# Optimization experiments

Hardware: AMD Instinct MI355X
Metric: run time of the kernel (lower is better)

Reference implementation:

```python
import jax, jax.numpy as jnp
import numpy as np

B, S, D, H = 2, 2048, 1024, 16
DK = D // H  # 64
SQRT_DK = DK ** 0.5
NEG = -1e9


def setup_inputs() -> dict:
    key = jax.random.key(0)
    ks = jax.random.split(key, 7)
    scale = 1.0 / np.sqrt(D)
    return {
        "x": jax.random.normal(ks[0], (B, S, D), jnp.float32),
        "encoder_output": jax.random.normal(ks[1], (B, S, D), jnp.float32),
        "mask": jax.random.randint(ks[2], (B, S), 0, 2, jnp.int32),
        "WQ": jax.random.normal(ks[3], (D, D), jnp.float32) * scale,
        "WK": jax.random.normal(ks[4], (D, D), jnp.float32) * scale,
        "WV": jax.random.normal(ks[5], (D, D), jnp.float32) * scale,
        "WO": jax.random.normal(ks[6], (D, D), jnp.float32) * scale,
    }


def reference(x, encoder_output, mask, WQ, WK, WV, WO):
    b, s, d = x.shape
    # project and split heads: (b, h, s, dk)
    q = (x @ WQ).reshape(b, s, H, DK).transpose(0, 2, 1, 3)
    k = (encoder_output @ WK).reshape(b, s, H, DK).transpose(0, 2, 1, 3)
    v = (encoder_output @ WV).reshape(b, s, H, DK).transpose(0, 2, 1, 3)
    # scores: (b, h, s_q, s_k)
    scores = jnp.einsum('bhqd,bhkd->bhqk', q, k) / SQRT_DK
    # future mask (strict upper triangle) + padding mask broadcast over key dim
    future = jnp.triu(jnp.ones((s, s), jnp.int32), 1)  # (s, s)
    m = mask[:, None, :, None] + future[None, None, :, :]  # (b, 1->h, s_q, s_k)
    scores = jnp.where(m != 0, NEG, scores)
    attn = jax.nn.softmax(scores, axis=-1)
    # context: (b, s, h, dk) -> (b, s, d)
    ctx = jnp.einsum('bhqk,bhkd->bqhd', attn, v).reshape(b, s, d)
    return ctx @ WO
```

## Files before the change

kernel.cpp:

```cpp
#include <hip/hip_runtime.h>
#include <hip/hip_bf16.h>

constexpr int B = 2, S = 2048, D = 1024, H = 16, DK = 64;
constexpr int M = B * S;
constexpr float LOG2E = 1.44269504088896f;
constexpr float NEGBIG = -3.0e38f;
constexpr float QSCALE = 0.125f * LOG2E;

using short8 = __attribute__((ext_vector_type(8))) short;
using short4v = __attribute__((ext_vector_type(4))) short;
using f32x4 = __attribute__((ext_vector_type(4))) float;

#define GLOBAL_AS __attribute__((address_space(1)))
#define LDS_AS __attribute__((address_space(3)))

__device__ __forceinline__ void gll16(const void* g, void* l) {
  __builtin_amdgcn_global_load_lds((const GLOBAL_AS void*)g, (LDS_AS void*)l, 16, 0, 0);
}

__device__ __forceinline__ short f2bf(float f) {
  __hip_bfloat16 h = __float2bfloat16(f);
  short s;
  __builtin_memcpy(&s, &h, 2);
  return s;
}
__device__ __forceinline__ unsigned pack2bf(float a, float b) {
  return (unsigned)(unsigned short)f2bf(a) | ((unsigned)(unsigned short)f2bf(b) << 16);
}

__global__ __launch_bounds__(256) void prep_kernel(const float* __restrict__ x,
                                                   const float* __restrict__ enc,
                                                   const float* __restrict__ W0,
                                                   const float* __restrict__ W1,
                                                   const float* __restrict__ W2,
                                                   const float* __restrict__ W3,
                                                   short* __restrict__ xb,
                                                   short* __restrict__ encb,
                                                   short* __restrict__ Wt) {
  __shared__ float t[64][65];
  const int bx = blockIdx.x;
  if (bx < 8192) {
    const float4* src = (const float4*)((bx & 4096) ? enc : x);
    short4v* dst = (short4v*)((bx & 4096) ? encb : xb);
    const int i = (bx & 4095) * 256 + threadIdx.x;
    const float4 v = src[i];
    short4v o;
    o[0] = f2bf(v.x); o[1] = f2bf(v.y); o[2] = f2bf(v.z); o[3] = f2bf(v.w);
    dst[i] = o;
  } else {
    const int idx = bx - 8192;
    const int z = idx >> 8, rem = idx & 255;
    const float* W = z == 0 ? W0 : z == 1 ? W1 : z == 2 ? W2 : W3;
    short* dstw = Wt + (size_t)z * D * D;
    const int n0 = (rem & 15) * 64, k0 = (rem >> 4) * 64;
    const int lx = threadIdx.x & 63, ly = threadIdx.x >> 6;
    #pragma unroll
    for (int r = 0; r < 64; r += 4)
      t[r + ly][lx] = W[(size_t)(k0 + r + ly) * D + n0 + lx];
    __syncthreads();
    #pragma unroll
    for (int r = 0; r < 64; r += 4)
      dstw[(size_t)(n0 + r + ly) * D + k0 + lx] = f2bf(t[lx][r + ly]);
  }
}

__global__ __launch_bounds__(512, 2) void gemm_qkv_kernel(const short* __restrict__ A0,
                                                          const short* __restrict__ A1,
                                                          const short* __restrict__ Wts,
                                                          short* __restrict__ Cv,
                                                          float* __restrict__ vsum) {
  __shared__ short As[2][4][256][8];
  __shared__ short Bs[2][4][256][8];
  const int z = blockIdx.z;
  const short* __restrict__ A = z ? A1 : A0;
  const short* __restrict__ Bt = Wts + (size_t)z * D * D;
  const float oscale = (z == 0) ? QSCALE : 1.0f;

  const int tid = threadIdx.x;
  const int lane = tid & 63, wid = tid >> 6;
  const int l15 = lane & 15, lg = lane >> 4;
  const int row0 = blockIdx.x * 256, col0 = blockIdx.y * 256;
  const int wm = wid >> 2, wn = wid & 3;
  f32x4 acc[8][4] = {};

  auto stage = [&](int k0, int nb) {
    #pragma unroll
    for (int it = 0; it < 2; ++it) {
      const int c = tid + it * 512;
      const int row = c & 255, kc2 = c >> 8;
      gll16(&A[(size_t)(row0 + row) * D + k0 + kc2 * 8],
            (char*)As + nb * 16384 + kc2 * 4096 + row * 16);
      gll16(&Bt[(size_t)(col0 + row) * D + k0 + kc2 * 8],
            (char*)Bs + nb * 16384 + kc2 * 4096 + row * 16);
    }
  };

  stage(0, 0);
  __syncthreads();
  int cur = 0;
  for (int t = 0; t < D / 32; ++t) {
    if (t < D / 32 - 1) stage((t + 1) * 32, cur ^ 1);
    short8 af[8], bfr[4];
    #pragma unroll
    for (int m = 0; m < 8; ++m) af[m] = *(const short8*)&As[cur][lg][wm * 128 + m * 16 + l15][0];
    #pragma unroll
    for (int n = 0; n < 4; ++n) bfr[n] = *(const short8*)&Bs[cur][lg][wn * 64 + n * 16 + l15][0];
    #pragma unroll
    for (int m = 0; m < 8; ++m)
      #pragma unroll
      for (int n = 0; n < 4; ++n)
        acc[m][n] = __builtin_amdgcn_mfma_f32_16x16x32_bf16(af[m], bfr[n], acc[m][n], 0, 0, 0);
    __syncthreads();
    cur ^= 1;
  }
  #pragma unroll
  for (int m = 0; m < 8; ++m) {
    #pragma unroll
    for (int r = 0; r < 4; ++r) {
      const int row = row0 + wm * 128 + m * 16 + 4 * lg + r;
      #pragma unroll
      for (int n = 0; n < 4; ++n) {
        const int col = col0 + wn * 64 + n * 16 + l15;
        Cv[(size_t)z * M * D + (size_t)row * D + col] = f2bf(acc[m][n][r] * oscale);
      }
    }
  }
  if (z == 2) {
    const int bidx = row0 >> 11;
    #pragma unroll
    for (int n = 0; n < 4; ++n) {
      float s = 0.f;
      #pragma unroll
      for (int m = 0; m < 8; ++m)
        s += acc[m][n][0] + acc[m][n][1] + acc[m][n][2] + acc[m][n][3];
      s += __shfl_xor(s, 16);
      s += __shfl_xor(s, 32);
      if (lg == 0) atomicAdd(&vsum[(size_t)bidx * D + col0 + wn * 64 + n * 16 + l15], s);
    }
  }
}

__global__ __launch_bounds__(256) void gemmO_kernel(const short* __restrict__ A,
                                                    const short* __restrict__ Bt,
                                                    float* __restrict__ C) {
  __shared__ short As[2][4][128][8];
  __shared__ short Bs[2][4][64][8];
  const int tid = threadIdx.x;
  const int lane = tid & 63, wid = tid >> 6;
  const int l15 = lane & 15, lg = lane >> 4;
  const int row0 = blockIdx.x * 128, col0 = blockIdx.y * 64;
  const int wm = wid >> 1, wn = wid & 1;
  f32x4 acc[4][2] = {};

  auto stage = [&](int k0, int nb) {
    #pragma unroll
    for (int it = 0; it < 2; ++it) {
      const int c = tid + it * 256;
      const int row = c & 127, kc2 = c >> 7;
      gll16(&A[(size_t)(row0 + row) * D + k0 + kc2 * 8],
            (char*)As + nb * 8192 + (wid * 64 + it * 256) * 16);
    }
    gll16(&Bt[(size_t)(col0 + lane) * D + k0 + wid * 8],
          (char*)Bs + nb * 4096 + wid * 1024);
  };

  stage(0, 0);
  __syncthreads();
  int cur = 0;
  for (int t = 0; t < D / 32; ++t) {
    if (t < D / 32 - 1) stage((t + 1) * 32, cur ^ 1);
    short8 af[4], bfr[2];
    #pragma unroll
    for (int m = 0; m < 4; ++m) af[m] = *(const short8*)&As[cur][lg][wm * 64 + m * 16 + l15][0];
    #pragma unroll
    for (int n = 0; n < 2; ++n) bfr[n] = *(const short8*)&Bs[cur][lg][wn * 32 + n * 16 + l15][0];
    #pragma unroll
    for (int m = 0; m < 4; ++m)
      #pragma unroll
      for (int n = 0; n < 2; ++n)
        acc[m][n] = __builtin_amdgcn_mfma_f32_16x16x32_bf16(af[m], bfr[n], acc[m][n], 0, 0, 0);
    __syncthreads();
    cur ^= 1;
  }
  #pragma unroll
  for (int m = 0; m < 4; ++m)
    #pragma unroll
    for (int r = 0; r < 4; ++r) {
      const int row = row0 + wm * 64 + m * 16 + 4 * lg + r;
      #pragma unroll
      for (int n = 0; n < 2; ++n)
        C[(size_t)row * D + col0 + wn * 32 + n * 16 + l15] = acc[m][n][r];
    }
}

__device__ __forceinline__ int keyof(int c, int i) {
  return ((c >> 1) << 5) + ((i >> 2) << 3) + ((c & 1) << 2) + (i & 3);
}
__device__ __forceinline__ int vt_byte(int kc, int d, int ksb) {
  return kc * 1024 + ((d ^ (kc & 7)) << 4) + ksb * 2;
}

__global__ __launch_bounds__(512, 4) void attn_kernel(const short* __restrict__ Qb,
                                                      const short* __restrict__ Kb,
                                                      const short* __restrict__ Vb,
                                                      const int* __restrict__ maskp,
                                                      const float* __restrict__ vsum,
                                                      short* __restrict__ ctxb) {
  __shared__ char KsBuf[2][16384];
  __shared__ char VtBuf[2][16384];
  const int bid = blockIdx.x;
  const int qt = (bid < 256) ? 15 - (bid >> 5) : (bid >> 5) - 8;
  const int bh = bid & 31;
  const int b = bh >> 4, h = bh & 15;
  const int tid = threadIdx.x, lane = tid & 63, wid = tid >> 6;
  const int l15 = lane & 15, lg = lane >> 4;
  const int ql = wid * 16 + l15;

  short8 qf[2];
  {
    const size_t o = (size_t)(b * S + qt * 128 + ql) * D + h * DK;
    qf[0] = *(const short8*)&Qb[o + lg * 8];
    qf[1] = *(const short8*)&Qb[o + 32 + lg * 8];
  }
  float m = NEGBIG, l = 0.f;
  f32x4 cx[4] = {};

  const int kkey = keyof(lg, l15);
  const int vu = tid & 63, dv = tid >> 6;
  const int vh = vu >> 5, vl = vu & 31;
  const int vkc = vl >> 2, vksb = (vl & 3) * 2;

  auto stageK = [&](int jc, int nb) {
    const size_t base = (size_t)(b * S + jc * 128 + kkey) * D + h * DK + wid * 8;
    gll16(&Kb[base], (char*)KsBuf + nb * 16384 + wid * 1024);
    gll16(&Kb[base + (size_t)64 * D], (char*)KsBuf + nb * 16384 + 8192 + wid * 1024);
  };
  auto loadV = [&](int jc, short8& va, short8& vb2) {
    const size_t vb0 = (size_t)(b * S + jc * 128 + 2 * vu) * D + h * DK + dv * 8;
    va = *(const short8*)&Vb[vb0];
    vb2 = *(const short8*)&Vb[vb0 + D];
  };
  auto writeV = [&](int nb, const short8& va, const short8& vb2) {
    char* dst = (char*)VtBuf + nb * 16384 + vh * 8192;
    #pragma unroll
    for (int i = 0; i < 8; ++i) {
      const unsigned w = (unsigned)(unsigned short)va[i] | ((unsigned)(unsigned short)vb2[i] << 16);
      *(unsigned*)(dst + vt_byte(vkc, dv * 8 + i, vksb)) = w;
    }
  };

  auto tile_pair = [&](int nb, bool do1, bool mask0, bool mask1) {
    const char* ks0 = (const char*)KsBuf + nb * 16384;
    const char* ks1 = ks0 + 8192;
    const char* vt0 = (const char*)VtBuf + nb * 16384;
    const char* vt1 = vt0 + 8192;
    f32x4 sa0[4], sa1[4];
    #pragma unroll
    for (int c = 0; c < 4; ++c) {
      const short8 kf0 = *(const short8*)(ks0 + lg * 1024 + c * 256 + l15 * 16);
      const short8 kf1 = *(const short8*)(ks0 + (4 + lg) * 1024 + c * 256 + l15 * 16);
      f32x4 zz = {0.f, 0.f, 0.f, 0.f};
      zz = __builtin_amdgcn_mfma_f32_16x16x32_bf16(kf0, qf[0], zz, 0, 0, 0);
      zz = __builtin_amdgcn_mfma_f32_16x16x32_bf16(kf1, qf[1], zz, 0, 0, 0);
      sa0[c] = zz;
    }
    if (do1) {
      #pragma unroll
      for (int c = 0; c < 4; ++c) {
        const short8 kf0 = *(const short8*)(ks1 + lg * 1024 + c * 256 + l15 * 16);
        const short8 kf1 = *(const short8*)(ks1 + (4 + lg) * 1024 + c * 256 + l15 * 16);
        f32x4 zz = {0.f, 0.f, 0.f, 0.f};
        zz = __builtin_amdgcn_mfma_f32_16x16x32_bf16(kf0, qf[0], zz, 0, 0, 0);
        zz = __builtin_amdgcn_mfma_f32_16x16x32_bf16(kf1, qf[1], zz, 0, 0, 0);
        sa1[c] = zz;
      }
    }
    if (mask0) {
      #pragma unroll
      for (int c = 0; c < 4; ++c)
        #pragma unroll
        for (int r = 0; r < 4; ++r)
          if (((c >> 1) << 5) + (lg << 3) + ((c & 1) << 2) + r > ql) sa0[c][r] = NEGBIG;
    }
    if (do1 && mask1) {
      #pragma unroll
      for (int c = 0; c < 4; ++c)
        #pragma unroll
        for (int r = 0; r < 4; ++r)
          if (64 + ((c >> 1) << 5) + (lg << 3) + ((c & 1) << 2) + r > ql) sa1[c][r] = NEGBIG;
    }
    float pm = sa0[0][0];
    #pragma unroll
    for (int c = 0; c < 4; ++c)
      #pragma unroll
      for (int r = 0; r < 4; ++r) pm = fmaxf(pm, sa0[c][r]);
    if (do1)
      #pragma unroll
      for (int c = 0; c < 4; ++c)
        #pragma unroll
        for (int r = 0; r < 4; ++r) pm = fmaxf(pm, sa1[c][r]);
    pm = fmaxf(pm, __shfl_xor(pm, 16));
    pm = fmaxf(pm, __shfl_xor(pm, 32));
    if (pm > m + 8.f) {
      const float sc = exp2f(m - pm);
      l *= sc;
      #pragma unroll
      for (int dt = 0; dt < 4; ++dt) cx[dt] *= sc;
      m = pm;
    }
    float rs = 0.f;
    #pragma unroll
    for (int c = 0; c < 4; ++c)
      #pragma unroll
      for (int r = 0; r < 4; ++r) {
        const float p = exp2f(sa0[c][r] - m);
        sa0[c][r] = p;
        rs += p;
      }
    if (do1)
      #pragma unroll
      for (int c = 0; c < 4; ++c)
        #pragma unroll
        for (int r = 0; r < 4; ++r) {
          const float p = exp2f(sa1[c][r] - m);
          sa1[c][r] = p;
          rs += p;
        }
    rs += __shfl_xor(rs, 16);
    rs += __shfl_xor(rs, 32);
    l += rs;
    {
      short8 pf[2];
      #pragma unroll
      for (int kk = 0; kk < 2; ++kk)
        #pragma unroll
        for (int jj = 0; jj < 8; ++jj)
          pf[kk][jj] = f2bf(sa0[kk * 2 + (jj >> 2)][jj & 3]);
      #pragma unroll
      for (int kk = 0; kk < 2; ++kk)
        #pragma unroll
        for (int dt = 0; dt < 4; ++dt) {
          const short8 vf = *(const short8*)(vt0 + vt_byte(kk * 4 + lg, dt * 16 + l15, 0));
          cx[dt] = __builtin_amdgcn_mfma_f32_16x16x32_bf16(vf, pf[kk], cx[dt], 0, 0, 0);
        }
    }
    if (do1) {
      short8 pf[2];
      #pragma unroll
      for (int kk = 0; kk < 2; ++kk)
        #pragma unroll
        for (int jj = 0; jj < 8; ++jj)
          pf[kk][jj] = f2bf(sa1[kk * 2 + (jj >> 2)][jj & 3]);
      #pragma unroll
      for (int kk = 0; kk < 2; ++kk)
        #pragma unroll
        for (int dt = 0; dt < 4; ++dt) {
          const short8 vf = *(const short8*)(vt1 + vt_byte(kk * 4 + lg, dt * 16 + l15, 0));
          cx[dt] = __builtin_amdgcn_mfma_f32_16x16x32_bf16(vf, pf[kk], cx[dt], 0, 0, 0);
        }
    }
  };

  {
    short8 va, vb2;
    stageK(0, 0);
    loadV(0, va, vb2);
    writeV(0, va, vb2);
  }
  __syncthreads();
  int cur = 0;
  for (int jc = 0; jc <= qt; ++jc) {
    short8 nva, nvb;
    if (jc < qt) { stageK(jc + 1, cur ^ 1); loadV(jc + 1, nva, nvb); }
    const bool diag = (jc == qt), hi = (wid >= 4);
    tile_pair(cur, !diag || hi, diag && !hi, diag && hi);
    if (jc < qt) writeV(cur ^ 1, nva, nvb);
    __syncthreads();
    cur ^= 1;
  }

  {
    const int qg = qt * 128 + ql;
    const int mq = maskp[b * S + qg];
    const float inv = 1.0f / l;
    constexpr float vscale = 1.0f / S;
    short* orow = &ctxb[(size_t)(b * S + qg) * D + h * DK];
    const float* vmb = &vsum[(size_t)b * D + h * DK];
    #pragma unroll
    for (int dt = 0; dt < 4; ++dt)
      #pragma unroll
      for (int p2 = 0; p2 < 2; ++p2) {
        const int d = dt * 16 + 4 * lg + p2 * 2;
        const float v0 = mq ? vmb[d] * vscale     : cx[dt][p2 * 2] * inv;
        const float v1 = mq ? vmb[d + 1] * vscale : cx[dt][p2 * 2 + 1] * inv;
        *(unsigned*)&orow[d] = pack2bf(v0, v1);
      }
  }
}

extern "C" void kernel_launch(void* const* d_in, const int* in_sizes, int n_in,
                              void* d_out, int out_size, void* d_ws, size_t ws_size,
                              hipStream_t stream) {
  (void)in_sizes; (void)n_in; (void)out_size; (void)ws_size;
  const float* x   = (const float*)d_in[0];
  const float* enc = (const float*)d_in[1];
  const int*   msk = (const int*)d_in[2];
  const float* WQ  = (const float*)d_in[3];
  const float* WK  = (const float*)d_in[4];
  const float* WV  = (const float*)d_in[5];
  const float* WO  = (const float*)d_in[6];
  float* out = (float*)d_out;

  char* ws = (char*)d_ws;
  const size_t MB = 1u << 20;
  short* xb    = (short*)(ws + 0);
  short* encb  = (short*)(ws + 8 * MB);
  short* Qb    = (short*)(ws + 16 * MB);
  short* WQt   = (short*)(ws + 40 * MB);
  float* vsum  = (float*)(ws + 48 * MB);
  short* Kb    = Qb + (size_t)M * D;
  short* Vb    = Kb + (size_t)M * D;
  short* WOt   = WQt + (size_t)3 * D * D;
  short* ctxb  = xb;

  hipMemsetAsync(vsum, 0, (size_t)B * D * sizeof(float), stream);

  prep_kernel<<<dim3(9216), 256, 0, stream>>>(x, enc, WQ, WK, WV, WO, xb, encb, WQt);

  gemm_qkv_kernel<<<dim3(M / 256, D / 256, 3), 512, 0, stream>>>(xb, encb, WQt, Qb, vsum);

  attn_kernel<<<dim3(512), 512, 0, stream>>>(Qb, Kb, Vb, msk, vsum, ctxb);

  gemmO_kernel<<<dim3(M / 128, D / 64), 256, 0, stream>>>(ctxb, WOt, out);
}
```

Measured before the change: 177.5 us.

## Restructure QKV GEMM into 8-phase half-tile pipeline with BK=64

Rewrites the QKV projection GEMM main loop to use K-tiles of 64 split into half-tiles per matrix, and moves to an 8-phase ping-pong schedule. Each phase loads fragments, issues the next half-tile's global-to-LDS copy, and runs MFMAs under raised priority with explicit vmcnt waits and barriers. Warp output tiles are reassigned to quadrants of the 256x256 block. The aim is to overlap global loads with MFMA work and cut per-iteration barrier overhead. In exchange it uses 128KB of LDS, which drops occupancy to one block per CU, and adds fragile hand-tuned wait counts.

```diff
diff --git a/kernel.cpp b/kernel.cpp
--- a/kernel.cpp
+++ b/kernel.cpp
@@ -69,8 +69,8 @@
                                                           const short* __restrict__ Wts,
                                                           short* __restrict__ Cv,
                                                           float* __restrict__ vsum) {
-  __shared__ short As[2][4][256][8];
-  __shared__ short Bs[2][4][256][8];
+  __shared__ char AsL[65536];
+  __shared__ char BsL[65536];
   const int z = blockIdx.z;
   const short* __restrict__ A = z ? A1 : A0;
   const short* __restrict__ Bt = Wts + (size_t)z * D * D;
@@ -83,60 +83,113 @@
   const int wm = wid >> 2, wn = wid & 3;
   f32x4 acc[8][4] = {};
 
-  auto stage = [&](int k0, int nb) {
+  auto stageH = [&](int mat, int sbuf, int half, int tile) {
+    const short* src = mat ? Bt : A;
+    const int base0 = mat ? col0 : row0;
+    char* dst = (mat ? BsL : AsL) + sbuf * 32768 + half * 16384;
+    const int k0 = tile * 64;
     #pragma unroll
     for (int it = 0; it < 2; ++it) {
       const int c = tid + it * 512;
-      const int row = c & 255, kc2 = c >> 8;
-      gll16(&A[(size_t)(row0 + row) * D + k0 + kc2 * 8],
-            (char*)As + nb * 16384 + kc2 * 4096 + row * 16);
-      gll16(&Bt[(size_t)(col0 + row) * D + k0 + kc2 * 8],
-            (char*)Bs + nb * 16384 + kc2 * 4096 + row * 16);
-    }
-  };
-
-  stage(0, 0);
-  __syncthreads();
-  int cur = 0;
-  for (int t = 0; t < D / 32; ++t) {
-    if (t < D / 32 - 1) stage((t + 1) * 32, cur ^ 1);
-    short8 af[8], bfr[4];
-    #pragma unroll
-    for (int m = 0; m < 8; ++m) af[m] = *(const short8*)&As[cur][lg][wm * 128 + m * 16 + l15][0];
-    #pragma unroll
-    for (int n = 0; n < 4; ++n) bfr[n] = *(const short8*)&Bs[cur][lg][wn * 64 + n * 16 + l15][0];
-    #pragma unroll
-    for (int m = 0; m < 8; ++m)
-      #pragma unroll
-      for (int n = 0; n < 4; ++n)
-        acc[m][n] = __builtin_amdgcn_mfma_f32_16x16x32_bf16(af[m], bfr[n], acc[m][n], 0, 0, 0);
-    __syncthreads();
-    cur ^= 1;
-  }
+      const int row = c & 127, kc = c >> 7;
+      gll16(&src[(size_t)(base0 + half * 128 + row) * D + k0 + kc * 8],
+            dst + kc * 2048 + row * 16);
+    }
+  };
+
+#define PHASE(RBUF, MH, NH, DOSTAGE, SMAT, SBUF, SH, STILE, VM)                            \
+  do {                                                                                     \
+    short8 af_[4][2], bv_[2][2];                                                           \
+    const char* ab_ = AsL + (RBUF) * 32768 + (MH) * 16384;                                 \
+    const char* bb_ = BsL + (RBUF) * 32768 + (NH) * 16384;                                 \
+    _Pragma("unroll") for (int m16 = 0; m16 < 4; ++m16)                                    \
+        _Pragma("unroll") for (int ks = 0; ks < 2; ++ks)                                   \
+            af_[m16][ks] = *(const short8*)(ab_ + (ks * 4 + lg) * 2048 +                   \
+                                            (wm * 64 + m16 * 16 + l15) * 16);              \
+    _Pragma("unroll") for (int n16 = 0; n16 < 2; ++n16)                                    \
+        _Pragma("unroll") for (int ks = 0; ks < 2; ++ks)                                   \
+            bv_[n16][ks] = *(const short8*)(bb_ + (ks * 4 + lg) * 2048 +                   \
+                                            (wn * 32 + n16 * 16 + l15) * 16);              \
+    if (DOSTAGE) stageH((SMAT), (SBUF), (SH), (STILE));                                    \
+    __builtin_amdgcn_s_barrier();                                                          \
+    asm volatile("s_waitcnt lgkmcnt(0)" ::: "memory");                                     \
+    __builtin_amdgcn_sched_barrier(0);                                                     \
+    __builtin_amdgcn_s_setprio(1);                                                         \
+    _Pragma("unroll") for (int m16 = 0; m16 < 4; ++m16)                                    \
+        _Pragma("unroll") for (int n16 = 0; n16 < 2; ++n16)                                \
+            _Pragma("unroll") for (int ks = 0; ks < 2; ++ks)                               \
+                acc[(MH) * 4 + m16][(NH) * 2 + n16] =                                      \
+                    __builtin_amdgcn_mfma_f32_16x16x32_bf16(                               \
+                        af_[m16][ks], bv_[n16][ks], acc[(MH) * 4 + m16][(NH) * 2 + n16],   \
+                        0, 0, 0);                                                          \
+    __builtin_amdgcn_s_setprio(0);                                                         \
+    if ((VM) == 4) asm volatile("s_waitcnt vmcnt(4)" ::: "memory");                        \
+    else if ((VM) == 0) asm volatile("s_waitcnt vmcnt(0)" ::: "memory");                   \
+    __builtin_amdgcn_s_barrier();                                                          \
+    __builtin_amdgcn_sched_barrier(0);                                                     \
+  } while (0)
+
+  stageH(0, 0, 0, 0);
+  stageH(1, 0, 0, 0);
+  stageH(0, 0, 1, 0);
+  stageH(1, 0, 1, 0);
+  stageH(0, 1, 0, 1);
+  stageH(1, 1, 0, 1);
+  asm volatile("s_waitcnt vmcnt(4)" ::: "memory");
+  __builtin_amdgcn_s_barrier();
+  __builtin_amdgcn_sched_barrier(0);
+
+  #pragma unroll 1
+  for (int i = 0; i < 8; ++i) {
+    const int tb = 2 * i + 1, ta2 = 2 * i + 2, tb2 = 2 * i + 3;
+    const bool pre = (i < 7);
+    const int vm = pre ? 4 : 0;
+    PHASE(0, 0, 0, true, 0, 1, 1, tb, -1);
+    PHASE(0, 0, 1, true, 1, 1, 1, tb, -1);
+    PHASE(0, 1, 0, pre, 0, 0, 0, ta2, -1);
+    PHASE(0, 1, 1, pre, 1, 0, 0, ta2, vm);
+    PHASE(1, 0, 0, pre, 0, 0, 1, ta2, -1);
+    PHASE(1, 0, 1, pre, 1, 0, 1, ta2, -1);
+    PHASE(1, 1, 0, pre, 0, 1, 0, tb2, -1);
+    PHASE(1, 1, 1, pre, 1, 1, 0, tb2, vm);
+  }
+#undef PHASE
+
   #pragma unroll
-  for (int m = 0; m < 8; ++m) {
-    #pragma unroll
-    for (int r = 0; r < 4; ++r) {
-      const int row = row0 + wm * 128 + m * 16 + 4 * lg + r;
-      #pragma unroll
-      for (int n = 0; n < 4; ++n) {
-        const int col = col0 + wn * 64 + n * 16 + l15;
-        Cv[(size_t)z * M * D + (size_t)row * D + col] = f2bf(acc[m][n][r] * oscale);
+  for (int mh = 0; mh < 2; ++mh)
+    #pragma unroll
+    for (int m16 = 0; m16 < 4; ++m16)
+      #pragma unroll
+      for (int r = 0; r < 4; ++r) {
+        const int row = row0 + mh * 128 + wm * 64 + m16 * 16 + 4 * lg + r;
+        #pragma unroll
+        for (int nh = 0; nh < 2; ++nh)
+          #pragma unroll
+          for (int n16 = 0; n16 < 2; ++n16) {
+            const int col = col0 + nh * 128 + wn * 32 + n16 * 16 + l15;
+            Cv[(size_t)z * M * D + (size_t)row * D + col] =
+                f2bf(acc[mh * 4 + m16][nh * 2 + n16][r] * oscale);
+          }
       }
-    }
-  }
   if (z == 2) {
     const int bidx = row0 >> 11;
     #pragma unroll
-    for (int n = 0; n < 4; ++n) {
-      float s = 0.f;
-      #pragma unroll
-      for (int m = 0; m < 8; ++m)
-        s += acc[m][n][0] + acc[m][n][1] + acc[m][n][2] + acc[m][n][3];
-      s += __shfl_xor(s, 16);
-      s += __shfl_xor(s, 32);
-      if (lg == 0) atomicAdd(&vsum[(size_t)bidx * D + col0 + wn * 64 + n * 16 + l15], s);
-    }
+    for (int nh = 0; nh < 2; ++nh)
+      #pragma unroll
+      for (int n16 = 0; n16 < 2; ++n16) {
+        float s = 0.f;
+        #pragma unroll
+        for (int mh = 0; mh < 2; ++mh)
+          #pragma unroll
+          for (int m16 = 0; m16 < 4; ++m16) {
+            const f32x4 a4 = acc[mh * 4 + m16][nh * 2 + n16];
+            s += a4[0] + a4[1] + a4[2] + a4[3];
+          }
+        s += __shfl_xor(s, 16);
+        s += __shfl_xor(s, 32);
+        if (lg == 0)
+          atomicAdd(&vsum[(size_t)bidx * D + col0 + nh * 128 + wn * 32 + n16 * 16 + l15], s);
+      }
   }
 }
 
```

After: 154.8 us. 1.15x faster.
